# Kernel optimization log

Hardware: AMD Instinct MI355X
Metric: run time of the kernel (lower is better)

## Reference

```python
import jax, jax.numpy as jnp
import numpy as np
from functools import partial

N_NODES = 20000
N_EDGES = 640000
HIDDEN = 64
BATCH = 8


def setup_inputs() -> dict:
    key = jax.random.key(0)
    k = jax.random.split(key, 6)
    x = jax.random.normal(k[0], (BATCH, N_NODES), dtype=jnp.float32)
    edge_index = jax.random.randint(k[1], (2, N_EDGES), 0, N_NODES, dtype=jnp.int64)
    edge_weight = jax.random.uniform(k[2], (N_EDGES,), dtype=jnp.float32)
    # GCNConv params (PyG default: glorot weight, zero bias)
    W1 = jax.random.normal(k[3], (1, HIDDEN), dtype=jnp.float32) * (1.0 / np.sqrt(1 + HIDDEN))
    b1 = jnp.zeros((HIDDEN,), dtype=jnp.float32)
    W2 = jax.random.normal(k[4], (HIDDEN, 1), dtype=jnp.float32) * (1.0 / np.sqrt(HIDDEN + 1))
    b2 = jnp.zeros((1,), dtype=jnp.float32)
    return {"x": x, "edge_index": edge_index, "edge_weight": edge_weight,
            "W1": W1, "b1": b1, "W2": W2, "b2": b2}


def _gcn_norm(edge_index, edge_weight, n_nodes):
    """PyG gcn_norm: add self-loops (weight 1), symmetric D^-1/2 A D^-1/2."""
    loop = jnp.arange(n_nodes, dtype=edge_index.dtype)
    row = jnp.concatenate([edge_index[0], loop])
    col = jnp.concatenate([edge_index[1], loop])
    ew = jnp.concatenate([edge_weight, jnp.ones((n_nodes,), edge_weight.dtype)])
    deg = jax.ops.segment_sum(ew, col, num_segments=n_nodes)  # [N]
    dis = jnp.where(deg > 0, jax.lax.rsqrt(jnp.where(deg > 0, deg, 1.0)), 0.0)
    norm = dis[row] * ew * dis[col]  # [E+N]
    return row, col, norm


def _gcn_conv(h, W, b, row, col, norm, n_nodes):
    # h: [B, N, Fin] -> [B, N, Fout]
    hW = h @ W                                   # [B, N, Fout]
    msg = hW[:, row, :] * norm[None, :, None]    # [B, E+N, Fout]
    agg = jax.vmap(partial(jax.ops.segment_sum, segment_ids=col,
                           num_segments=n_nodes))(msg)
    return agg + b


def reference(x, edge_index, edge_weight, W1, b1, W2, b2):
    n_nodes = x.shape[1]
    row, col, norm = _gcn_norm(edge_index, edge_weight, n_nodes)
    h = x[..., None]                                        # [B, N, 1]
    h = jax.nn.relu(_gcn_conv(h, W1, b1, row, col, norm, n_nodes))
    # dropout(p=0.2) is identity in eval mode
    delta = _gcn_conv(h, W2, b2, row, col, norm, n_nodes)[..., 0]  # [B, N]
    return x + 0.5 * delta
```

## Files before the change

### kernel.cpp

```cpp
#include <hip/hip_runtime.h>

#define N_NODES 20000
#define N_EDGES 640000
#define HIDDEN  64
#define BATCH   8
#define NBLK_G  512
#define SLICE   (N_EDGES / NBLK_G)
#define NBUCK   256
#define MAXCOLS 80
#define CAP     80

typedef unsigned long long ull;

__device__ inline int wave_iscan(int v, int lane) {
#pragma unroll
    for (int off = 1; off < 64; off <<= 1) {
        int u = __shfl_up(v, off, 64);
        if (lane >= off) v += u;
    }
    return v;
}

__device__ inline int bucket_base(int k) { return (k * N_NODES + NBUCK - 1) >> 8; }

__global__ void k_group(const int* __restrict__ row, const int* __restrict__ col,
                        const float* __restrict__ ew,
                        ull* __restrict__ gbuf, int* __restrict__ cnt,
                        int* __restrict__ locoff) {
    __shared__ ull recs[SLICE];
    __shared__ unsigned char bks[SLICE];
    __shared__ int bcnt[NBUCK];
    __shared__ int bcur[NBUCK];
    __shared__ int ws4[4];
    int b = blockIdx.x, tid = threadIdx.x;
    bcnt[tid] = 0;
    __syncthreads();
    int ebase = b * SLICE;
    for (int j = tid; j < SLICE; j += 256) {
        int e = ebase + j;
        int r = row[e], c = col[e];
        int k = (c * NBUCK) / N_NODES;
        int cl = c - bucket_base(k);
        recs[j] = ((ull)(unsigned)((r << 7) | cl) << 32) | (ull)__float_as_uint(ew[e]);
        bks[j] = (unsigned char)k;
        atomicAdd(&bcnt[k], 1);
    }
    __syncthreads();
    int lane = tid & 63, wid = tid >> 6;
    int v = bcnt[tid];
    int incl = wave_iscan(v, lane);
    if (lane == 63) ws4[wid] = incl;
    __syncthreads();
    if (tid == 0) {
        int r0 = 0;
#pragma unroll
        for (int w = 0; w < 4; ++w) { int s = ws4[w]; ws4[w] = r0; r0 += s; }
    }
    __syncthreads();
    int excl = incl - v + ws4[wid];
    cnt[b * NBUCK + tid]    = v;
    locoff[b * NBUCK + tid] = excl;
    bcur[tid] = excl;
    __syncthreads();
    for (int j = tid; j < SLICE; j += 256) {
        int k = bks[j];
        int pos = atomicAdd(&bcur[k], 1);
        gbuf[ebase + pos] = recs[j];
    }
}

__global__ void k_place(const int* __restrict__ cnt, const int* __restrict__ locoff,
                        const ull* __restrict__ gbuf,
                        const float* __restrict__ x,
                        int* __restrict__ outcnt, float* __restrict__ dis,
                        float* __restrict__ xT, ull* __restrict__ sedge) {
    __shared__ int colcur[MAXCOLS];
    __shared__ unsigned degfx[MAXCOLS];
    int k = blockIdx.x, tid = threadIdx.x;
    int cbase = bucket_base(k);
    int sz = bucket_base(k + 1) - cbase;
    if (tid < MAXCOLS) { colcur[tid] = 0; degfx[tid] = 0u; }
    __syncthreads();
    int len = cnt[tid * NBUCK + k];
    const ull* src = gbuf + tid * SLICE + locoff[tid * NBUCK + k];
    for (int i = 0; i < len; ++i) {
        ull rec = src[i];
        unsigned hi = (unsigned)(rec >> 32);
        int cl = hi & 127;
        int r  = (int)(hi >> 7);
        float w = __uint_as_float((unsigned)rec);
        int rank = atomicAdd(&colcur[cl], 1);
        atomicAdd(&degfx[cl], (unsigned)(w * 16777216.0f + 0.5f));
        if (rank < CAP)
            sedge[(ull)(cbase + cl) * CAP + rank] =
                ((ull)(unsigned)r << 32) | (ull)(unsigned)rec;
    }
    __syncthreads();
    if (tid < sz) {
        int c = cbase + tid;
        outcnt[c] = colcur[tid];
        dis[c] = rsqrtf((float)degfx[tid] * 5.9604644775390625e-8f + 1.0f);
    }
    for (int u = tid; u < sz * BATCH; u += 512) {
        int ci = u >> 3, b = u & 7;
        int c = cbase + ci;
        xT[(c << 3) + b] = x[b * N_NODES + c];
    }
}

__global__ void k_gather1(const int* __restrict__ cnt, const ull* __restrict__ sedge,
                          const float* __restrict__ xT, const float* __restrict__ dis,
                          const float* __restrict__ W1, const float* __restrict__ b1,
                          const float* __restrict__ W2, const float* __restrict__ b2,
                          float* __restrict__ t, int N) {
    int i = blockIdx.x * blockDim.x + threadIdx.x;
    if (i >= N * 32) return;
    int n = i >> 5;
    int w = i & 31, k = w >> 3, b = w & 7;
    int len = cnt[n]; if (len > CAP) len = CAP;
    int j0 = (len * k) >> 2;
    int j1 = (len * (k + 1)) >> 2;
    const ull* sl = sedge + (ull)n * CAP;
    float s = 0.0f;
    for (int j = j0; j < j1; ++j) {
        ull v = sl[j];
        int r = (int)(v >> 32);
        float wgt = __uint_as_float((unsigned)v);
        s = fmaf(dis[r] * wgt, xT[(r << 3) + b], s);
    }
    s += __shfl_xor(s, 8, 64);
    s += __shfl_xor(s, 16, 64);
    float di = dis[n];
    s = di * fmaf(di, xT[(n << 3) + b], s);
    float acc = 0.0f;
#pragma unroll
    for (int ff = 0; ff < 16; ++ff) {
        int f = (k << 4) + ff;
        float h = fmaf(s, W1[f], b1[f]);
        acc = fmaf(fmaxf(h, 0.0f), W2[f], acc);
    }
    acc += __shfl_xor(acc, 8, 64);
    acc += __shfl_xor(acc, 16, 64);
    if (k == 0) t[(n << 3) + b] = acc;
}

__global__ void k_gather2(const int* __restrict__ cnt, const ull* __restrict__ sedge,
                          const float* __restrict__ t, const float* __restrict__ xT,
                          const float* __restrict__ dis, const float* __restrict__ b2,
                          float* __restrict__ out, int N) {
    int i = blockIdx.x * blockDim.x + threadIdx.x;
    if (i >= N * 32) return;
    int n = i >> 5;
    int w = i & 31, k = w >> 3, b = w & 7;
    int len = cnt[n]; if (len > CAP) len = CAP;
    int j0 = (len * k) >> 2;
    int j1 = (len * (k + 1)) >> 2;
    const ull* sl = sedge + (ull)n * CAP;
    float g = 0.0f;
    for (int j = j0; j < j1; ++j) {
        ull v = sl[j];
        int r = (int)(v >> 32);
        float wgt = __uint_as_float((unsigned)v);
        g = fmaf(dis[r] * wgt, t[(r << 3) + b], g);
    }
    g += __shfl_xor(g, 8, 64);
    g += __shfl_xor(g, 16, 64);
    if (k == 0) {
        float di = dis[n];
        g = di * fmaf(di, t[(n << 3) + b], g);
        out[b * N + n] = xT[(n << 3) + b] + 0.5f * (b2[0] + g);
    }
}

extern "C" void kernel_launch(void* const* d_in, const int* in_sizes, int n_in,
                              void* d_out, int out_size, void* d_ws, size_t ws_size,
                              hipStream_t stream) {
    const float* x  = (const float*)d_in[0];
    const int*   ei = (const int*)d_in[1];
    const float* ew = (const float*)d_in[2];
    const float* W1 = (const float*)d_in[3];
    const float* b1 = (const float*)d_in[4];
    const float* W2 = (const float*)d_in[5];
    const float* b2 = (const float*)d_in[6];
    float* out = (float*)d_out;

    const int N = N_NODES, E = N_EDGES;
    const int* row = ei;
    const int* col = ei + E;

    ull*   gbuf   = (ull*)d_ws;
    ull*   sedge  = gbuf + E;
    float* xT     = (float*)(sedge + (ull)N * CAP);
    float* t      = xT + N * BATCH;
    int*   cnt    = (int*)(t + N * BATCH);
    int*   locoff = cnt + NBLK_G * NBUCK;
    int*   outcnt = locoff + NBLK_G * NBUCK;
    float* dis    = (float*)(outcnt + N);

    const int BS = 256;
    int gS = (N * 32 + BS - 1) / BS;

    k_group  <<<NBLK_G, 256, 0, stream>>>(row, col, ew, gbuf, cnt, locoff);
    k_place  <<<NBUCK,  512, 0, stream>>>(cnt, locoff, gbuf, x, outcnt, dis, xT, sedge);
    k_gather1<<<gS,     BS,  0, stream>>>(outcnt, sedge, xT, dis, W1, b1, W2, b2, t, N);
    k_gather2<<<gS,     BS,  0, stream>>>(outcnt, sedge, t, xT, dis, b2, out, N);
}
```

Baseline: 53.24 us.

## Pack edges into 32-bit records and pre-scale features by source degree norm

Edge records shrink from 64 to 32 bits by packing the 15-bit source index with a 17-bit quantized edge weight. The source-side dis[r] factor is folded into pre-scaled feature arrays (xd = dis*x, td = dis*t), so each gather does one load and one FMA instead of an extra dis[r] lookup. The goal is to cut gather memory traffic and random loads in both aggregation kernels. In exchange, edge weights are quantized to about 1e-5 precision, which could affect accuracy tolerance, and k_place gains an extra array write and a barrier.

```diff
diff --git a/kernel.cpp b/kernel.cpp
--- a/kernel.cpp
+++ b/kernel.cpp
@@ -9,6 +9,8 @@
 #define NBUCK   256
 #define MAXCOLS 80
 #define CAP     80
+#define NORM_SCALE 131071.0f
+#define NORM_INV   7.62945274e-6f
 
 typedef unsigned long long ull;
 
@@ -73,9 +75,11 @@
                         const ull* __restrict__ gbuf,
                         const float* __restrict__ x,
                         int* __restrict__ outcnt, float* __restrict__ dis,
-                        float* __restrict__ xT, ull* __restrict__ sedge) {
+                        float* __restrict__ xT, float* __restrict__ xd,
+                        unsigned* __restrict__ sedge) {
     __shared__ int colcur[MAXCOLS];
     __shared__ unsigned degfx[MAXCOLS];
+    __shared__ float sdis[MAXCOLS];
     int k = blockIdx.x, tid = threadIdx.x;
     int cbase = bucket_base(k);
     int sz = bucket_base(k + 1) - cbase;
@@ -91,28 +95,33 @@
         float w = __uint_as_float((unsigned)rec);
         int rank = atomicAdd(&colcur[cl], 1);
         atomicAdd(&degfx[cl], (unsigned)(w * 16777216.0f + 0.5f));
+        unsigned q = (unsigned)(w * NORM_SCALE + 0.5f);
         if (rank < CAP)
-            sedge[(ull)(cbase + cl) * CAP + rank] =
-                ((ull)(unsigned)r << 32) | (ull)(unsigned)rec;
+            sedge[(cbase + cl) * CAP + rank] = ((unsigned)r << 17) | q;
     }
     __syncthreads();
     if (tid < sz) {
         int c = cbase + tid;
         outcnt[c] = colcur[tid];
-        dis[c] = rsqrtf((float)degfx[tid] * 5.9604644775390625e-8f + 1.0f);
-    }
+        float d = rsqrtf((float)degfx[tid] * 5.9604644775390625e-8f + 1.0f);
+        dis[c] = d;
+        sdis[tid] = d;
+    }
+    __syncthreads();
     for (int u = tid; u < sz * BATCH; u += 512) {
         int ci = u >> 3, b = u & 7;
         int c = cbase + ci;
-        xT[(c << 3) + b] = x[b * N_NODES + c];
-    }
-}
-
-__global__ void k_gather1(const int* __restrict__ cnt, const ull* __restrict__ sedge,
-                          const float* __restrict__ xT, const float* __restrict__ dis,
+        float xv = x[b * N_NODES + c];
+        xT[(c << 3) + b] = xv;
+        xd[(c << 3) + b] = sdis[ci] * xv;
+    }
+}
+
+__global__ void k_gather1(const int* __restrict__ cnt, const unsigned* __restrict__ sedge,
+                          const float* __restrict__ xd, const float* __restrict__ dis,
                           const float* __restrict__ W1, const float* __restrict__ b1,
                           const float* __restrict__ W2, const float* __restrict__ b2,
-                          float* __restrict__ t, int N) {
+                          float* __restrict__ td, int N) {
     int i = blockIdx.x * blockDim.x + threadIdx.x;
     if (i >= N * 32) return;
     int n = i >> 5;
@@ -120,18 +129,17 @@
     int len = cnt[n]; if (len > CAP) len = CAP;
     int j0 = (len * k) >> 2;
     int j1 = (len * (k + 1)) >> 2;
-    const ull* sl = sedge + (ull)n * CAP;
+    const unsigned* sl = sedge + n * CAP;
     float s = 0.0f;
     for (int j = j0; j < j1; ++j) {
-        ull v = sl[j];
-        int r = (int)(v >> 32);
-        float wgt = __uint_as_float((unsigned)v);
-        s = fmaf(dis[r] * wgt, xT[(r << 3) + b], s);
+        unsigned v = sl[j];
+        float wq = (float)(v & 0x1FFFFu) * NORM_INV;
+        s = fmaf(wq, xd[(int)((v >> 17) << 3) + b], s);
     }
     s += __shfl_xor(s, 8, 64);
     s += __shfl_xor(s, 16, 64);
     float di = dis[n];
-    s = di * fmaf(di, xT[(n << 3) + b], s);
+    s = di * (s + xd[(n << 3) + b]);
     float acc = 0.0f;
 #pragma unroll
     for (int ff = 0; ff < 16; ++ff) {
@@ -141,11 +149,11 @@
     }
     acc += __shfl_xor(acc, 8, 64);
     acc += __shfl_xor(acc, 16, 64);
-    if (k == 0) t[(n << 3) + b] = acc;
-}
-
-__global__ void k_gather2(const int* __restrict__ cnt, const ull* __restrict__ sedge,
-                          const float* __restrict__ t, const float* __restrict__ xT,
+    if (k == 0) td[(n << 3) + b] = di * acc;
+}
+
+__global__ void k_gather2(const int* __restrict__ cnt, const unsigned* __restrict__ sedge,
+                          const float* __restrict__ td, const float* __restrict__ xT,
                           const float* __restrict__ dis, const float* __restrict__ b2,
                           float* __restrict__ out, int N) {
     int i = blockIdx.x * blockDim.x + threadIdx.x;
@@ -155,19 +163,18 @@
     int len = cnt[n]; if (len > CAP) len = CAP;
     int j0 = (len * k) >> 2;
     int j1 = (len * (k + 1)) >> 2;
-    const ull* sl = sedge + (ull)n * CAP;
+    const unsigned* sl = sedge + n * CAP;
     float g = 0.0f;
     for (int j = j0; j < j1; ++j) {
-        ull v = sl[j];
-        int r = (int)(v >> 32);
-        float wgt = __uint_as_float((unsigned)v);
-        g = fmaf(dis[r] * wgt, t[(r << 3) + b], g);
+        unsigned v = sl[j];
+        float wq = (float)(v & 0x1FFFFu) * NORM_INV;
+        g = fmaf(wq, td[(int)((v >> 17) << 3) + b], g);
     }
     g += __shfl_xor(g, 8, 64);
     g += __shfl_xor(g, 16, 64);
     if (k == 0) {
         float di = dis[n];
-        g = di * fmaf(di, t[(n << 3) + b], g);
+        g = di * (g + td[(n << 3) + b]);
         out[b * N + n] = xT[(n << 3) + b] + 0.5f * (b2[0] + g);
     }
 }
@@ -188,20 +195,21 @@
     const int* row = ei;
     const int* col = ei + E;
 
-    ull*   gbuf   = (ull*)d_ws;
-    ull*   sedge  = gbuf + E;
-    float* xT     = (float*)(sedge + (ull)N * CAP);
-    float* t      = xT + N * BATCH;
-    int*   cnt    = (int*)(t + N * BATCH);
-    int*   locoff = cnt + NBLK_G * NBUCK;
-    int*   outcnt = locoff + NBLK_G * NBUCK;
-    float* dis    = (float*)(outcnt + N);
+    ull*      gbuf   = (ull*)d_ws;
+    unsigned* sedge  = (unsigned*)(gbuf + E);
+    float*    xT     = (float*)(sedge + N * CAP);
+    float*    xd     = xT + N * BATCH;
+    float*    td     = xd + N * BATCH;
+    int*      cnt    = (int*)(td + N * BATCH);
+    int*      locoff = cnt + NBLK_G * NBUCK;
+    int*      outcnt = locoff + NBLK_G * NBUCK;
+    float*    dis    = (float*)(outcnt + N);
 
     const int BS = 256;
     int gS = (N * 32 + BS - 1) / BS;
 
     k_group  <<<NBLK_G, 256, 0, stream>>>(row, col, ew, gbuf, cnt, locoff);
-    k_place  <<<NBUCK,  512, 0, stream>>>(cnt, locoff, gbuf, x, outcnt, dis, xT, sedge);
-    k_gather1<<<gS,     BS,  0, stream>>>(outcnt, sedge, xT, dis, W1, b1, W2, b2, t, N);
-    k_gather2<<<gS,     BS,  0, stream>>>(outcnt, sedge, t, xT, dis, b2, out, N);
-}
+    k_place  <<<NBUCK,  512, 0, stream>>>(cnt, locoff, gbuf, x, outcnt, dis, xT, xd, sedge);
+    k_gather1<<<gS,     BS,  0, stream>>>(outcnt, sedge, xd, dis, W1, b1, W2, b2, td, N);
+    k_gather2<<<gS,     BS,  0, stream>>>(outcnt, sedge, td, xT, dis, b2, out, N);
+}
```

Measured after the change: 49.19 us. 7.6% less time.
